# Optimization experiments

Hardware: AMD Instinct MI355X
Metric: run time of the kernel (lower is better)

## Reference

```python
import jax, jax.numpy as jnp
import numpy as np

N_SRC = 100000
N_DST = 100000
N_EDGES = 640000
D = 128
D_OUT = 128


def setup_inputs() -> dict:
    key = jax.random.key(0)
    k1, k2, k3, k4, k5, k6 = jax.random.split(key, 6)
    h_src = jax.random.normal(k1, (N_SRC, D), dtype=jnp.float32)
    h_dst = jax.random.normal(k2, (N_DST, D), dtype=jnp.float32)
    src_idx = jax.random.randint(k3, (N_EDGES,), 0, N_SRC, dtype=jnp.int32)
    dst_idx = jax.random.randint(k4, (N_EDGES,), 0, N_DST, dtype=jnp.int32)
    W = jax.random.normal(k5, (2 * D, D_OUT), dtype=jnp.float32) * 0.05
    b = jax.random.normal(k6, (D_OUT,), dtype=jnp.float32) * 0.05
    return {"h_src": h_src, "h_dst": h_dst, "src_idx": src_idx,
            "dst_idx": dst_idx, "W": W, "b": b}


def reference(h_src, h_dst, src_idx, dst_idx, W, b):
    # copy_u: gather source features along edges -> [E, D]
    msgs = h_src[src_idx]
    # mean aggregation per destination node (segment mean)
    summed = jax.ops.segment_sum(msgs, dst_idx, num_segments=N_DST)  # [N_dst, D]
    deg = jax.ops.segment_sum(jnp.ones((N_EDGES,), dtype=h_src.dtype),
                              dst_idx, num_segments=N_DST)  # [N_dst]
    h_N = summed / jnp.maximum(deg, 1.0)[:, None]
    # concat self + neighbor mean, then linear projection
    h_total = jnp.concatenate([h_dst, h_N], axis=1)  # [N_dst, 2D]
    return h_total @ W + b
```

## Files before the change

kernel.cpp:

```cpp
#include <hip/hip_runtime.h>

#define D 128
#define N_SRC 100000
#define N_DST 100000
#define N_EDGES 640000

#define SCAN_BLK 1024
#define N_SCAN_BLOCKS ((N_DST + SCAN_BLK - 1) / SCAN_BLK)

#define SCAT_BLOCKS ((N_EDGES + 255) / 256)
#define CVT_BLOCKS  ((N_SRC * D / 8) / 256)
#define PACKW_BLOCKS 128

typedef __attribute__((ext_vector_type(8))) short s8v;
typedef __attribute__((ext_vector_type(4))) float f32x4;

__device__ __forceinline__ unsigned short f2bf(float f) {
    unsigned int u = __float_as_uint(f);
    u += 0x7fffu + ((u >> 16) & 1u);
    return (unsigned short)(u >> 16);
}

__device__ __forceinline__ unsigned int pk2(float a, float b) {
    return (unsigned int)f2bf(a) | ((unsigned int)f2bf(b) << 16);
}

__global__ __launch_bounds__(256) void hist_kernel(
    const int* __restrict__ dst_idx, int* __restrict__ counts)
{
    int e = blockIdx.x * 256 + threadIdx.x;
    if (e < N_EDGES) atomicAdd(&counts[dst_idx[e]], 1);
}

__global__ __launch_bounds__(256) void scan_blocks(
    const int* __restrict__ counts, int* __restrict__ row_start,
    int* __restrict__ block_sums)
{
    __shared__ int sh[256];
    const int tid = threadIdx.x;
    const int base = blockIdx.x * SCAN_BLK + tid * 4;
    int v[4];
    int local = 0;
#pragma unroll
    for (int k = 0; k < 4; k++) {
        int idx = base + k;
        v[k] = (idx < N_DST) ? counts[idx] : 0;
        local += v[k];
    }
    sh[tid] = local;
    __syncthreads();
    for (int off = 1; off < 256; off <<= 1) {
        int t = (tid >= off) ? sh[tid - off] : 0;
        __syncthreads();
        sh[tid] += t;
        __syncthreads();
    }
    int run = (tid == 0) ? 0 : sh[tid - 1];
    if (tid == 255) block_sums[blockIdx.x] = sh[255];
#pragma unroll
    for (int k = 0; k < 4; k++) {
        int idx = base + k;
        if (idx < N_DST) row_start[idx] = run;
        run += v[k];
    }
}

__global__ __launch_bounds__(256) void add_offsets(
    int* __restrict__ row_start, const int* __restrict__ block_sums,
    int* __restrict__ cursor)
{
    __shared__ int sh[128];
    const int tid = threadIdx.x;
    if (tid < 128) sh[tid] = (tid < N_SCAN_BLOCKS) ? block_sums[tid] : 0;
    __syncthreads();
    for (int off = 1; off < 128; off <<= 1) {
        int t = (tid < 128 && tid >= off) ? sh[tid - off] : 0;
        __syncthreads();
        if (tid < 128) sh[tid] += t;
        __syncthreads();
    }
    int i = blockIdx.x * 256 + tid;
    if (i < N_DST) {
        int blk = i / SCAN_BLK;
        int off = (blk == 0) ? 0 : sh[blk - 1];
        int v = row_start[i] + off;
        row_start[i] = v;
        cursor[i] = v;
    }
    if (i == 0) row_start[N_DST] = N_EDGES;
}

__global__ __launch_bounds__(256) void scatter_cvt(
    const int* __restrict__ src_idx, const int* __restrict__ dst_idx,
    int* __restrict__ cursor, int* __restrict__ edge_src,
    const float* __restrict__ h_src, unsigned int* __restrict__ mir32,
    const float* __restrict__ W, unsigned short* __restrict__ Bp)
{
    const int blk = blockIdx.x;
    const int tid = threadIdx.x;
    if (blk < SCAT_BLOCKS) {
        int e = blk * 256 + tid;
        if (e < N_EDGES) {
            int d = dst_idx[e];
            int pos = atomicAdd(&cursor[d], 1);
            edge_src[pos] = src_idx[e];
        }
    } else if (blk < SCAT_BLOCKS + CVT_BLOCKS) {
        int id = (blk - SCAT_BLOCKS) * 256 + tid;
        const float4* p = (const float4*)(h_src + (size_t)id * 8);
        float4 x = p[0], y = p[1];
        uint4 o;
        o.x = pk2(x.x, x.y); o.y = pk2(x.z, x.w);
        o.z = pk2(y.x, y.y); o.w = pk2(y.z, y.w);
        *(uint4*)(mir32 + (size_t)(id >> 4) * 64 + (id & 15) * 4) = o;
    } else {
        int id = (blk - SCAT_BLOCKS - CVT_BLOCKS) * 256 + tid;
        if (id < 32768) {
            int j = id & 7;
            int l = (id >> 3) & 63;
            int t = (id >> 9) & 7;
            int s = id >> 12;
            int k = s * 32 + (l >> 4) * 8 + j;
            int n = t * 16 + (l & 15);
            Bp[id] = f2bf(W[k * D + n]);
        }
    }
}

__global__ __launch_bounds__(64, 8) void fused_ag(
    const float* __restrict__ h_dst,
    const unsigned short* __restrict__ mir,
    const int* __restrict__ row_start,
    const int* __restrict__ edge_src,
    const unsigned short* __restrict__ Bp,
    const float* __restrict__ bias,
    float* __restrict__ out)
{
    __shared__ uint4 hN4[256];
    char* hN = (char*)hN4;

    const int lane = threadIdx.x;
    const int quad = lane >> 4;
    const int lr = lane & 15;
    const int rw0 = blockIdx.x * 16;

#pragma unroll
    for (int i = 0; i < 4; i++) {
        int rl = i * 4 + quad;
        int row = rw0 + rl;
        int start = row_start[row];
        int deg = row_start[row + 1] - start;
        int nfull = deg & ~7;
        float a[8] = {0.f, 0.f, 0.f, 0.f, 0.f, 0.f, 0.f, 0.f};
        for (int base = 0; base < nfull; base += 8) {
#pragma unroll
            for (int t = 0; t < 8; t++) {
                int s = edge_src[start + base + t];
                uint4 u = *(const uint4*)(mir + (size_t)s * 128 + lr * 8);
                a[0] += __uint_as_float(u.x << 16);
                a[1] += __uint_as_float(u.x & 0xffff0000u);
                a[2] += __uint_as_float(u.y << 16);
                a[3] += __uint_as_float(u.y & 0xffff0000u);
                a[4] += __uint_as_float(u.z << 16);
                a[5] += __uint_as_float(u.z & 0xffff0000u);
                a[6] += __uint_as_float(u.w << 16);
                a[7] += __uint_as_float(u.w & 0xffff0000u);
            }
        }
        if (nfull < deg) {
#pragma unroll
            for (int t = 0; t < 8; t++) {
                int s = edge_src[start + min(nfull + t, deg - 1)];
                uint4 u = *(const uint4*)(mir + (size_t)s * 128 + lr * 8);
                float m = ((nfull + t) < deg) ? 1.f : 0.f;
                a[0] = fmaf(__uint_as_float(u.x << 16), m, a[0]);
                a[1] = fmaf(__uint_as_float(u.x & 0xffff0000u), m, a[1]);
                a[2] = fmaf(__uint_as_float(u.y << 16), m, a[2]);
                a[3] = fmaf(__uint_as_float(u.y & 0xffff0000u), m, a[3]);
                a[4] = fmaf(__uint_as_float(u.z << 16), m, a[4]);
                a[5] = fmaf(__uint_as_float(u.z & 0xffff0000u), m, a[5]);
                a[6] = fmaf(__uint_as_float(u.w << 16), m, a[6]);
                a[7] = fmaf(__uint_as_float(u.w & 0xffff0000u), m, a[7]);
            }
        }
        float inv = 1.0f / fmaxf((float)deg, 1.0f);
        uint4 o;
        o.x = pk2(a[0] * inv, a[1] * inv);
        o.y = pk2(a[2] * inv, a[3] * inv);
        o.z = pk2(a[4] * inv, a[5] * inv);
        o.w = pk2(a[6] * inv, a[7] * inv);
        int ba = (rl * 256 + lr * 16) ^ ((rl & 7) << 4);
        *(uint4*)(hN + ba) = o;
    }

    s8v an[4];
    {
        int rl = lr;
#pragma unroll
        for (int s = 0; s < 4; s++) {
            int ba = (rl * 256 + s * 64 + quad * 16) ^ ((rl & 7) << 4);
            an[s] = *(const s8v*)(hN + ba);
        }
    }

    const int r0 = rw0 + lr;
    const float* p0 = h_dst + (size_t)r0 * D + quad * 8;
    float4 x0[4], y0[4];
#pragma unroll
    for (int s = 0; s < 4; s++) {
        x0[s] = *(const float4*)(p0 + s * 32);
        y0[s] = *(const float4*)(p0 + s * 32 + 4);
    }
    s8v af0[4];
#pragma unroll
    for (int s = 0; s < 4; s++) {
        unsigned short u0[8];
        u0[0]=f2bf(x0[s].x); u0[1]=f2bf(x0[s].y); u0[2]=f2bf(x0[s].z); u0[3]=f2bf(x0[s].w);
        u0[4]=f2bf(y0[s].x); u0[5]=f2bf(y0[s].y); u0[6]=f2bf(y0[s].z); u0[7]=f2bf(y0[s].w);
        af0[s] = *(s8v*)u0;
    }

    f32x4 acc[8];
#pragma unroll
    for (int t = 0; t < 8; t++) acc[t] = (f32x4){0.f, 0.f, 0.f, 0.f};

#pragma unroll
    for (int s = 0; s < 8; s++) {
        s8v a0 = (s < 4) ? af0[s] : an[s - 4];
#pragma unroll
        for (int t = 0; t < 8; t++) {
            s8v bf = *(const s8v*)(Bp + ((size_t)(s * 8 + t) * 64 + lane) * 8);
            acc[t] = __builtin_amdgcn_mfma_f32_16x16x32_bf16(a0, bf, acc[t], 0, 0, 0);
        }
    }

#pragma unroll
    for (int t = 0; t < 8; t++) {
        float bv = bias[t * 16 + lr];
#pragma unroll
        for (int r = 0; r < 4; r++) {
            int row = rw0 + quad * 4 + r;
            out[(size_t)row * D + t * 16 + lr] = acc[t][r] + bv;
        }
    }
}

extern "C" void kernel_launch(void* const* d_in, const int* in_sizes, int n_in,
                              void* d_out, int out_size, void* d_ws, size_t ws_size,
                              hipStream_t stream) {
    const float* h_src  = (const float*)d_in[0];
    const float* h_dst  = (const float*)d_in[1];
    const int* src_idx  = (const int*)d_in[2];
    const int* dst_idx  = (const int*)d_in[3];
    const float* W      = (const float*)d_in[4];
    const float* b      = (const float*)d_in[5];
    float* out = (float*)d_out;

    unsigned short* Bp = (unsigned short*)d_ws;
    int* ws_i          = (int*)((char*)d_ws + 65536);
    int* row_start     = ws_i;
    int* cursor        = row_start + (N_DST + 1);
    int* counts        = cursor + N_DST;
    int* block_sums    = counts + N_DST;
    int* edge_src      = block_sums + N_SCAN_BLOCKS;

    size_t int_bytes = (size_t)(N_DST + 1 + N_DST + N_DST + N_SCAN_BLOCKS
                                + N_EDGES) * 4;
    size_t mir_off   = (65536 + int_bytes + 255) & ~(size_t)255;
    unsigned short* mir = (unsigned short*)((char*)d_ws + mir_off);

    hipMemsetAsync(counts, 0, (size_t)N_DST * sizeof(int), stream);

    hist_kernel<<<(N_EDGES + 255) / 256, 256, 0, stream>>>(dst_idx, counts);
    scan_blocks<<<N_SCAN_BLOCKS, 256, 0, stream>>>(counts, row_start, block_sums);
    add_offsets<<<(N_DST + 255) / 256, 256, 0, stream>>>(row_start, block_sums, cursor);

    scatter_cvt<<<SCAT_BLOCKS + CVT_BLOCKS + PACKW_BLOCKS, 256, 0, stream>>>(
        src_idx, dst_idx, cursor, edge_src,
        h_src, (unsigned int*)mir, W, Bp);

    fused_ag<<<N_DST / 16, 64, 0, stream>>>(
        h_dst, mir, row_start, edge_src, Bp, b, out);
}
```

Measured before the change: 267.3 us.

## Gather neighbor rows via global_load_lds into LDS, one row per wave

Restructures the neighbor aggregation so the whole wave handles one destination row at a time. It loads up to 32 edge indices cooperatively, broadcasts them with shuffles, and issues async global-to-LDS loads for 4 neighbor rows per instruction. Each lane then accumulates two bf16 columns from LDS. The h_dst load and conversion are hoisted ahead of the gather. The change aims to raise memory-level parallelism and cut per-lane VGPR use, but it adds a full vmcnt(0) wait per 32-edge chunk, serial per-row processing, and extra LDS traffic.

```diff
diff --git a/kernel.cpp b/kernel.cpp
--- a/kernel.cpp
+++ b/kernel.cpp
@@ -127,7 +127,7 @@
     }
 }
 
-__global__ __launch_bounds__(64, 8) void fused_ag(
+__global__ __launch_bounds__(64) void fused_ag(
     const float* __restrict__ h_dst,
     const unsigned short* __restrict__ mir,
     const int* __restrict__ row_start,
@@ -136,88 +136,61 @@
     const float* __restrict__ bias,
     float* __restrict__ out)
 {
-    __shared__ uint4 hN4[256];
-    char* hN = (char*)hN4;
+    __shared__ unsigned int gbuf[32 * 64];
+    __shared__ char hN[4096];
 
     const int lane = threadIdx.x;
     const int quad = lane >> 4;
     const int lr = lane & 15;
     const int rw0 = blockIdx.x * 16;
 
-#pragma unroll
-    for (int i = 0; i < 4; i++) {
-        int rl = i * 4 + quad;
-        int row = rw0 + rl;
-        int start = row_start[row];
-        int deg = row_start[row + 1] - start;
-        int nfull = deg & ~7;
-        float a[8] = {0.f, 0.f, 0.f, 0.f, 0.f, 0.f, 0.f, 0.f};
-        for (int base = 0; base < nfull; base += 8) {
-#pragma unroll
-            for (int t = 0; t < 8; t++) {
-                int s = edge_src[start + base + t];
-                uint4 u = *(const uint4*)(mir + (size_t)s * 128 + lr * 8);
-                a[0] += __uint_as_float(u.x << 16);
-                a[1] += __uint_as_float(u.x & 0xffff0000u);
-                a[2] += __uint_as_float(u.y << 16);
-                a[3] += __uint_as_float(u.y & 0xffff0000u);
-                a[4] += __uint_as_float(u.z << 16);
-                a[5] += __uint_as_float(u.z & 0xffff0000u);
-                a[6] += __uint_as_float(u.w << 16);
-                a[7] += __uint_as_float(u.w & 0xffff0000u);
+    const float* p0 = h_dst + (size_t)(rw0 + lr) * D + quad * 8;
+    s8v af0[4];
+#pragma unroll
+    for (int s = 0; s < 4; s++) {
+        float4 x = *(const float4*)(p0 + s * 32);
+        float4 y = *(const float4*)(p0 + s * 32 + 4);
+        unsigned short u0[8];
+        u0[0]=f2bf(x.x); u0[1]=f2bf(x.y); u0[2]=f2bf(x.z); u0[3]=f2bf(x.w);
+        u0[4]=f2bf(y.x); u0[5]=f2bf(y.y); u0[6]=f2bf(y.z); u0[7]=f2bf(y.w);
+        af0[s] = *(s8v*)u0;
+    }
+
+    for (int r = 0; r < 16; ++r) {
+        const int row = rw0 + r;
+        const int start = __builtin_amdgcn_readfirstlane(row_start[row]);
+        const int deg = __builtin_amdgcn_readfirstlane(row_start[row + 1]) - start;
+        float a0 = 0.f, a1 = 0.f;
+        for (int cb = 0; cb < deg; cb += 32) {
+            const int cnt = min(deg - cb, 32);
+            int vid = edge_src[start + min(cb + lane, deg - 1)];
+            for (int e = 0; e < cnt; e += 4) {
+                int s = __shfl(vid, e + quad);
+                const char* gp = (const char*)mir + ((size_t)s * 256 + lr * 16);
+                __builtin_amdgcn_global_load_lds(
+                    (const __attribute__((address_space(1))) void*)gp,
+                    (__attribute__((address_space(3))) void*)&gbuf[e * 64],
+                    16, 0, 0);
             }
-        }
-        if (nfull < deg) {
-#pragma unroll
-            for (int t = 0; t < 8; t++) {
-                int s = edge_src[start + min(nfull + t, deg - 1)];
-                uint4 u = *(const uint4*)(mir + (size_t)s * 128 + lr * 8);
-                float m = ((nfull + t) < deg) ? 1.f : 0.f;
-                a[0] = fmaf(__uint_as_float(u.x << 16), m, a[0]);
-                a[1] = fmaf(__uint_as_float(u.x & 0xffff0000u), m, a[1]);
-                a[2] = fmaf(__uint_as_float(u.y << 16), m, a[2]);
-                a[3] = fmaf(__uint_as_float(u.y & 0xffff0000u), m, a[3]);
-                a[4] = fmaf(__uint_as_float(u.z << 16), m, a[4]);
-                a[5] = fmaf(__uint_as_float(u.z & 0xffff0000u), m, a[5]);
-                a[6] = fmaf(__uint_as_float(u.w << 16), m, a[6]);
-                a[7] = fmaf(__uint_as_float(u.w & 0xffff0000u), m, a[7]);
+            asm volatile("s_waitcnt vmcnt(0)" ::: "memory");
+            __builtin_amdgcn_sched_barrier(0);
+            for (int e = 0; e < cnt; ++e) {
+                unsigned int u = gbuf[e * 64 + lane];
+                a0 += __uint_as_float(u << 16);
+                a1 += __uint_as_float(u & 0xffff0000u);
             }
         }
-        float inv = 1.0f / fmaxf((float)deg, 1.0f);
-        uint4 o;
-        o.x = pk2(a[0] * inv, a[1] * inv);
-        o.y = pk2(a[2] * inv, a[3] * inv);
-        o.z = pk2(a[4] * inv, a[5] * inv);
-        o.w = pk2(a[6] * inv, a[7] * inv);
-        int ba = (rl * 256 + lr * 16) ^ ((rl & 7) << 4);
-        *(uint4*)(hN + ba) = o;
+        const float inv = 1.0f / fmaxf((float)deg, 1.0f);
+        unsigned int pw = pk2(a0 * inv, a1 * inv);
+        int ba = (r * 256 + lane * 4) ^ ((r & 7) << 4);
+        *(unsigned int*)(hN + ba) = pw;
     }
 
     s8v an[4];
-    {
-        int rl = lr;
-#pragma unroll
-        for (int s = 0; s < 4; s++) {
-            int ba = (rl * 256 + s * 64 + quad * 16) ^ ((rl & 7) << 4);
-            an[s] = *(const s8v*)(hN + ba);
-        }
-    }
-
-    const int r0 = rw0 + lr;
-    const float* p0 = h_dst + (size_t)r0 * D + quad * 8;
-    float4 x0[4], y0[4];
 #pragma unroll
     for (int s = 0; s < 4; s++) {
-        x0[s] = *(const float4*)(p0 + s * 32);
-        y0[s] = *(const float4*)(p0 + s * 32 + 4);
-    }
-    s8v af0[4];
-#pragma unroll
-    for (int s = 0; s < 4; s++) {
-        unsigned short u0[8];
-        u0[0]=f2bf(x0[s].x); u0[1]=f2bf(x0[s].y); u0[2]=f2bf(x0[s].z); u0[3]=f2bf(x0[s].w);
-        u0[4]=f2bf(y0[s].x); u0[5]=f2bf(y0[s].y); u0[6]=f2bf(y0[s].z); u0[7]=f2bf(y0[s].w);
-        af0[s] = *(s8v*)u0;
+        int ba = (lr * 256 + s * 64 + quad * 16) ^ ((lr & 7) << 4);
+        an[s] = *(const s8v*)(hN + ba);
     }
 
     f32x4 acc[8];
```

Measured after the change: 297.7 us. 1.11x slower.
